# Performance work log

Measured on AMD Instinct MI355X. Metric: run time of the kernel, lower is better.

Reference implementation:

```python
import jax, jax.numpy as jnp
import numpy as np

B, T, D, H = 2, 2048, 2048, 16
HD = D // H  # head_dim = 128


def setup_inputs() -> dict:
    key = jax.random.key(0)
    ks = jax.random.split(key, 7)
    s = 1.0 / np.sqrt(D)
    return {
        "x": jax.random.normal(ks[0], (B, T, D), jnp.float32),
        "Wq": jax.random.normal(ks[1], (D, D), jnp.float32) * s,
        "Wk": jax.random.normal(ks[2], (D, D), jnp.float32) * s,
        "Wv": jax.random.normal(ks[3], (D, D), jnp.float32) * s,
        "Wo": jax.random.normal(ks[4], (D, D), jnp.float32) * s,
        "rope_cos": jax.random.uniform(ks[5], (T, HD), jnp.float32, -1.0, 1.0),
        "rope_sin": jax.random.uniform(ks[6], (T, HD), jnp.float32, -1.0, 1.0),
    }


def _rope(x, cos, sin):
    # x: [B,H,T,HD]; cos/sin: [T,HD] broadcast over batch/heads
    half = x.shape[-1] // 2
    lhs, rhs = x[..., :half], x[..., half:]
    rotated = jnp.concatenate((-rhs, lhs), axis=-1)
    return cos[None, None] * x + rotated * sin[None, None]


def reference(x, Wq, Wk, Wv, Wo, rope_cos, rope_sin):
    Bc, Tc, Dc = x.shape
    # torch nn.Linear: y = x @ W.T
    q = (x @ Wq.T).reshape(Bc, Tc, H, HD).transpose(0, 2, 1, 3)
    k = (x @ Wk.T).reshape(Bc, Tc, H, HD).transpose(0, 2, 1, 3)
    v = (x @ Wv.T).reshape(Bc, Tc, H, HD).transpose(0, 2, 1, 3)
    q = _rope(q, rope_cos[:Tc], rope_sin[:Tc])
    k = _rope(k, rope_cos[:Tc], rope_sin[:Tc])
    scores = jnp.einsum('bhqd,bhkd->bhqk', q, k) / jnp.sqrt(jnp.float32(HD))
    causal = jnp.triu(jnp.ones((Tc, Tc), bool), k=1)
    scores = jnp.where(causal[None, None], -jnp.inf, scores)
    attn = jax.nn.softmax(scores, axis=-1)
    ctx = jnp.einsum('bhqk,bhkd->bhqd', attn, v)
    ctx = ctx.transpose(0, 2, 1, 3).reshape(Bc, Tc, Dc)
    return ctx @ Wo.T
```

## Files before the change

kernel.cpp:

```cpp
#include <hip/hip_runtime.h>

typedef __attribute__((ext_vector_type(4))) float   f32x4;
typedef __attribute__((ext_vector_type(8))) __bf16  bf16x8;
typedef __attribute__((ext_vector_type(4))) __bf16  bf16x4;
typedef __attribute__((ext_vector_type(8))) unsigned short u16x8;

#define NH   16
#define HD   128
#define TSEQ 2048
#define DM   2048
#define MT   4096

__device__ __forceinline__ f32x4 mfma_bf16(bf16x8 a, bf16x8 b, f32x4 c) {
  return __builtin_amdgcn_mfma_f32_16x16x32_bf16(a, b, c, 0, 0, 0);
}

__device__ __forceinline__ void gl_lds16(const __bf16* g, __bf16* l) {
  __builtin_amdgcn_global_load_lds(
      (const __attribute__((address_space(1))) void*)g,
      (__attribute__((address_space(3))) void*)l, 16, 0, 0);
}

__global__ __launch_bounds__(256) void k_cvt(const float* __restrict__ s,
                                             __bf16* __restrict__ d, int n4) {
  int i = blockIdx.x * 256 + threadIdx.x;
  int stride = gridDim.x * 256;
  for (; i < n4; i += stride) {
    f32x4 v = ((const f32x4*)s)[i];
    bf16x4 o;
    o[0] = (__bf16)v[0]; o[1] = (__bf16)v[1];
    o[2] = (__bf16)v[2]; o[3] = (__bf16)v[3];
    ((bf16x4*)d)[i] = o;
  }
}

__global__ __launch_bounds__(256) void k_cvtw(
    const float* __restrict__ W0, const float* __restrict__ W1,
    const float* __restrict__ W2, const float* __restrict__ W3,
    __bf16* __restrict__ D0, __bf16* __restrict__ D1,
    __bf16* __restrict__ D2, __bf16* __restrict__ D3, int n4) {
  int z = blockIdx.z;
  const float* s = (z == 0) ? W0 : (z == 1) ? W1 : (z == 2) ? W2 : W3;
  __bf16*      d = (z == 0) ? D0 : (z == 1) ? D1 : (z == 2) ? D2 : D3;
  int i = blockIdx.x * 256 + threadIdx.x;
  int stride = gridDim.x * 256;
  for (; i < n4; i += stride) {
    f32x4 v = ((const f32x4*)s)[i];
    bf16x4 o;
    o[0] = (__bf16)v[0]; o[1] = (__bf16)v[1];
    o[2] = (__bf16)v[2]; o[3] = (__bf16)v[3];
    ((bf16x4*)d)[i] = o;
  }
}

template <int MODE>
__global__ __launch_bounds__(256) void k_gemm(
    const __bf16* __restrict__ A,
    const __bf16* __restrict__ B0, const __bf16* __restrict__ B1,
    const __bf16* __restrict__ B2,
    __bf16* __restrict__ D0, __bf16* __restrict__ D1, __bf16* __restrict__ D2,
    float* __restrict__ F) {
  __shared__ __bf16 As[128 * 32];
  __shared__ __bf16 Bs[128 * 32];

  const __bf16* __restrict__ Bm;
  __bf16* Dst = nullptr;
  if (MODE == 1) {
    int z = blockIdx.z;
    Bm  = (z == 0) ? B0 : (z == 1 ? B1 : B2);
    Dst = (z == 0) ? D0 : (z == 1 ? D1 : D2);
  } else {
    Bm = B0;
  }

  const int bid = blockIdx.x;
  const int wg  = (bid & 7) * 64 + (bid >> 3);
  const int n0  = (wg & 15) * 128;
  const int m0  = (wg >> 4) * 128;

  const int tid  = threadIdx.x;
  const int lane = tid & 63, w = tid >> 6;
  const int g    = lane >> 4, li = lane & 15;
  const int wr   = w >> 1, wc = w & 1;
  const int srow = lane >> 2;
  const int sseg = lane & 3;

  const f32x4 zero = {0.f, 0.f, 0.f, 0.f};
  f32x4 acc[4][4];
#pragma unroll
  for (int i = 0; i < 4; i++)
#pragma unroll
    for (int j = 0; j < 4; j++) acc[i][j] = zero;

  for (int k0 = 0; k0 < DM; k0 += 32) {
#pragma unroll
    for (int c = 0; c < 2; c++) {
      const int ch = w * 2 + c;
      gl_lds16(&A[(size_t)(m0 + ch * 16 + srow) * DM + k0 + sseg * 8],
               &As[ch * 512]);
      gl_lds16(&Bm[(size_t)(n0 + ch * 16 + srow) * DM + k0 + sseg * 8],
               &Bs[ch * 512]);
    }
    __syncthreads();
    bf16x8 af[4], bfr[4];
#pragma unroll
    for (int i = 0; i < 4; i++)
      af[i] = *(const bf16x8*)&As[(wr * 64 + i * 16 + li) * 32 + g * 8];
#pragma unroll
    for (int i = 0; i < 4; i++)
      bfr[i] = *(const bf16x8*)&Bs[(wc * 64 + i * 16 + li) * 32 + g * 8];
#pragma unroll
    for (int mi = 0; mi < 4; mi++)
#pragma unroll
      for (int ni = 0; ni < 4; ni++)
        acc[mi][ni] = mfma_bf16(af[mi], bfr[ni], acc[mi][ni]);
    __syncthreads();
  }

#pragma unroll
  for (int mi = 0; mi < 4; mi++)
#pragma unroll
    for (int ni = 0; ni < 4; ni++) {
      int colb = n0 + wc * 64 + ni * 16 + li;
#pragma unroll
      for (int r = 0; r < 4; r++) {
        int rowb = m0 + wr * 64 + mi * 16 + g * 4 + r;
        float vv = acc[mi][ni][r];
        if (MODE == 0) {
          F[(size_t)rowb * DM + colb] = vv;
        } else {
          int h = colb >> 7, d = colb & 127;
          int b = rowb >> 11, t = rowb & 2047;
          Dst[(((size_t)(b * NH + h)) * TSEQ + t) * HD + d] = (__bf16)vv;
        }
      }
    }
}

__global__ __launch_bounds__(256) void k_rope(__bf16* __restrict__ q,
                                              __bf16* __restrict__ kk,
                                              const float* __restrict__ rc,
                                              const float* __restrict__ rs) {
  int gid    = blockIdx.x * 256 + threadIdx.x;
  int tensor = gid >> 20;
  int rem    = gid & ((1 << 20) - 1);
  int bh     = rem >> 15;
  int r2     = rem & 32767;
  int t      = r2 >> 4;
  int j      = r2 & 15;
  int d0     = j * 4;
  __bf16* base = (tensor ? kk : q) + ((size_t)bh * TSEQ + t) * HD;
  f32x4 ca = *(const f32x4*)&rc[t * HD + d0];
  f32x4 cb = *(const f32x4*)&rc[t * HD + d0 + 64];
  f32x4 sa = *(const f32x4*)&rs[t * HD + d0];
  f32x4 sb = *(const f32x4*)&rs[t * HD + d0 + 64];
  bf16x4 xa = *(bf16x4*)&base[d0];
  bf16x4 xb = *(bf16x4*)&base[d0 + 64];
  bf16x4 oa, ob;
#pragma unroll
  for (int u = 0; u < 4; u++) {
    float fa = (float)xa[u], fb = (float)xb[u];
    oa[u] = (__bf16)(ca[u] * fa - fb * sa[u]);
    ob[u] = (__bf16)(cb[u] * fb + fa * sb[u]);
  }
  *(bf16x4*)&base[d0]      = oa;
  *(bf16x4*)&base[d0 + 64] = ob;
}

__global__ __launch_bounds__(256) void k_trans(const __bf16* __restrict__ v,
                                               __bf16* __restrict__ vt) {
  __shared__ unsigned short tile[64][73];
  int bh = blockIdx.z;
  int t0 = blockIdx.x * 64, d0 = blockIdx.y * 64;
  int tid = threadIdx.x;
  int r = tid >> 2, s4 = tid & 3;
  const unsigned short* src =
      (const unsigned short*)v + ((size_t)bh * TSEQ + t0) * HD + d0;
  u16x8 a = *(const u16x8*)&src[(size_t)r * HD + s4 * 16];
  u16x8 b = *(const u16x8*)&src[(size_t)r * HD + s4 * 16 + 8];
#pragma unroll
  for (int u = 0; u < 8; u++) {
    tile[r][s4 * 16 + u]     = a[u];
    tile[r][s4 * 16 + 8 + u] = b[u];
  }
  __syncthreads();
  unsigned short* dst =
      (unsigned short*)vt + ((size_t)bh * HD + d0) * TSEQ + t0;
  u16x8 o1, o2;
#pragma unroll
  for (int u = 0; u < 8; u++) {
    o1[u] = tile[s4 * 16 + u][r];
    o2[u] = tile[s4 * 16 + 8 + u][r];
  }
  *(u16x8*)&dst[(size_t)r * TSEQ + s4 * 16]     = o1;
  *(u16x8*)&dst[(size_t)r * TSEQ + s4 * 16 + 8] = o2;
}

__global__ __launch_bounds__(256, 2) void k_attn(const __bf16* __restrict__ q,
                                                 const __bf16* __restrict__ k,
                                                 const __bf16* __restrict__ vt,
                                                 __bf16* __restrict__ ctx) {
  __shared__ __bf16 Ks[64 * 136];
  __shared__ __bf16 Vs[128 * 72];
  __shared__ __bf16 Ps[4][32 * 72];

  const int bid = blockIdx.x;
  const int wg  = (bid & 7) * 64 + (bid >> 3);
  const int bh  = wg >> 4;
  const int qt  = 15 - (wg & 15);
  const int q0  = qt * 128;

  const int tid  = threadIdx.x;
  const int lane = tid & 63, w = tid >> 6;
  const int g    = lane >> 4, li = lane & 15;
  const int qw   = q0 + w * 32;

  const __bf16* qb = q  + (size_t)bh * TSEQ * HD;
  const __bf16* kb = k  + (size_t)bh * TSEQ * HD;
  const __bf16* vb = vt + (size_t)bh * HD * TSEQ;

  const float CST = 0.08838834764831845f * 1.4426950408889634f;
  bf16x8 qf[2][4];
#pragma unroll
  for (int s = 0; s < 2; s++)
#pragma unroll
    for (int kc = 0; kc < 4; kc++) {
      bf16x8 t =
          *(const bf16x8*)&qb[(size_t)(qw + s * 16 + li) * HD + kc * 32 + g * 8];
      bf16x8 o;
#pragma unroll
      for (int e = 0; e < 8; e++) o[e] = (__bf16)((float)t[e] * CST);
      qf[s][kc] = o;
    }

  const f32x4 zero = {0.f, 0.f, 0.f, 0.f};
  f32x4 o[2][8];
#pragma unroll
  for (int s = 0; s < 2; s++)
#pragma unroll
    for (int dt = 0; dt < 8; dt++) o[s][dt] = zero;
  float mrow[2][4], lrow[2][4];
#pragma unroll
  for (int s = 0; s < 2; s++)
#pragma unroll
    for (int r = 0; r < 4; r++) { mrow[s][r] = -1e30f; lrow[s][r] = 0.f; }

  const int nkt = 2 * qt + 2;

  const int kR = tid >> 4, kS = tid & 15;
  const int vR = tid >> 3, vS = tid & 7;

  bf16x8 pk[4], pv[4];
#pragma unroll
  for (int i = 0; i < 4; i++) {
    pk[i] = *(const bf16x8*)&kb[(size_t)(kR + 16 * i) * HD + kS * 8];
    pv[i] = *(const bf16x8*)&vb[(size_t)(vR + 32 * i) * TSEQ + vS * 8];
  }

  for (int kt = 0; kt < nkt; kt++) {
    const int kv0 = kt * 64;
    __syncthreads();
#pragma unroll
    for (int i = 0; i < 4; i++)
      *(bf16x8*)&Ks[(kR + 16 * i) * 136 + kS * 8] = pk[i];
#pragma unroll
    for (int i = 0; i < 4; i++)
      *(bf16x8*)&Vs[(vR + 32 * i) * 72 + vS * 8] = pv[i];
    if (kt + 1 < nkt) {
      const int nv0 = kv0 + 64;
#pragma unroll
      for (int i = 0; i < 4; i++) {
        pk[i] = *(const bf16x8*)&kb[(size_t)(nv0 + kR + 16 * i) * HD + kS * 8];
        pv[i] = *(const bf16x8*)&vb[(size_t)(vR + 32 * i) * TSEQ + nv0 + vS * 8];
      }
    }
    __syncthreads();

    if (kv0 <= qw + 31) {
      f32x4 sc[2][4];
#pragma unroll
      for (int s = 0; s < 2; s++)
#pragma unroll
        for (int kvf = 0; kvf < 4; kvf++) sc[s][kvf] = zero;
#pragma unroll
      for (int kvf = 0; kvf < 4; kvf++)
#pragma unroll
        for (int kc = 0; kc < 4; kc++) {
          bf16x8 kf =
              *(const bf16x8*)&Ks[(kvf * 16 + li) * 136 + kc * 32 + g * 8];
          sc[0][kvf] = mfma_bf16(qf[0][kc], kf, sc[0][kvf]);
          sc[1][kvf] = mfma_bf16(qf[1][kc], kf, sc[1][kvf]);
        }
      if (kv0 + 63 > qw) {
#pragma unroll
        for (int s = 0; s < 2; s++)
#pragma unroll
          for (int kvf = 0; kvf < 4; kvf++) {
            int kg = kv0 + kvf * 16 + li;
#pragma unroll
            for (int r = 0; r < 4; r++) {
              int qg = qw + s * 16 + g * 4 + r;
              if (kg > qg) sc[s][kvf][r] = -1e30f;
            }
          }
      }
      float mnew[2][4];
      bool upd = false;
#pragma unroll
      for (int s = 0; s < 2; s++)
#pragma unroll
        for (int r = 0; r < 4; r++) {
          float a = fmaxf(fmaxf(sc[s][0][r], sc[s][1][r]),
                          fmaxf(sc[s][2][r], sc[s][3][r]));
          a = fmaxf(a, __shfl_xor(a, 1));
          a = fmaxf(a, __shfl_xor(a, 2));
          a = fmaxf(a, __shfl_xor(a, 4));
          a = fmaxf(a, __shfl_xor(a, 8));
          mnew[s][r] = fmaxf(mrow[s][r], a);
          upd = upd || (a > mrow[s][r]);
        }
      if (__any(upd)) {
#pragma unroll
        for (int s = 0; s < 2; s++)
#pragma unroll
          for (int r = 0; r < 4; r++) {
            float fac = __builtin_amdgcn_exp2f(mrow[s][r] - mnew[s][r]);
            mrow[s][r] = mnew[s][r];
            lrow[s][r] *= fac;
#pragma unroll
            for (int dt = 0; dt < 8; dt++) o[s][dt][r] *= fac;
          }
      }
#pragma unroll
      for (int s = 0; s < 2; s++)
#pragma unroll
        for (int kvf = 0; kvf < 4; kvf++) {
#pragma unroll
          for (int r = 0; r < 4; r++) {
            float p = __builtin_amdgcn_exp2f(sc[s][kvf][r] - mrow[s][r]);
            lrow[s][r] += p;
            Ps[w][(s * 16 + g * 4 + r) * 72 + kvf * 16 + li] = (__bf16)p;
          }
        }
      bf16x8 pa[2][2];
#pragma unroll
      for (int s = 0; s < 2; s++)
#pragma unroll
        for (int kvs = 0; kvs < 2; kvs++)
          pa[s][kvs] =
              *(const bf16x8*)&Ps[w][(s * 16 + li) * 72 + kvs * 32 + g * 8];
#pragma unroll
      for (int dt = 0; dt < 8; dt++) {
        bf16x8 v0 = *(const bf16x8*)&Vs[(dt * 16 + li) * 72 + g * 8];
        bf16x8 v1 = *(const bf16x8*)&Vs[(dt * 16 + li) * 72 + 32 + g * 8];
        o[0][dt] = mfma_bf16(pa[0][0], v0, o[0][dt]);
        o[0][dt] = mfma_bf16(pa[0][1], v1, o[0][dt]);
        o[1][dt] = mfma_bf16(pa[1][0], v0, o[1][dt]);
        o[1][dt] = mfma_bf16(pa[1][1], v1, o[1][dt]);
      }
    }
  }

  const int b = bh >> 4, h = bh & 15;
#pragma unroll
  for (int s = 0; s < 2; s++)
#pragma unroll
    for (int r = 0; r < 4; r++) {
      float l = lrow[s][r];
      l += __shfl_xor(l, 1);
      l += __shfl_xor(l, 2);
      l += __shfl_xor(l, 4);
      l += __shfl_xor(l, 8);
      float inv = 1.0f / l;
      size_t rowoff =
          ((size_t)(b * TSEQ + qw + s * 16 + g * 4 + r)) * DM + h * HD;
#pragma unroll
      for (int dt = 0; dt < 8; dt++)
        ctx[rowoff + dt * 16 + li] = (__bf16)(o[s][dt][r] * inv);
    }
}

extern "C" void kernel_launch(void* const* d_in, const int* in_sizes, int n_in,
                              void* d_out, int out_size, void* d_ws,
                              size_t ws_size, hipStream_t stream) {
  const float* x  = (const float*)d_in[0];
  const float* Wq = (const float*)d_in[1];
  const float* Wk = (const float*)d_in[2];
  const float* Wv = (const float*)d_in[3];
  const float* Wo = (const float*)d_in[4];
  const float* rc = (const float*)d_in[5];
  const float* rs = (const float*)d_in[6];
  float* out = (float*)d_out;

  __bf16* xb   = (__bf16*)d_ws;
  __bf16* wqb  = xb  + (size_t)MT * DM;
  __bf16* wkb  = wqb + (size_t)DM * DM;
  __bf16* wvb  = wkb + (size_t)DM * DM;
  __bf16* wob  = wvb + (size_t)DM * DM;
  __bf16* qbuf = wob + (size_t)DM * DM;
  __bf16* kbuf = qbuf + (size_t)MT * DM;
  __bf16* vbuf = kbuf + (size_t)MT * DM;
  __bf16* vtb  = vbuf + (size_t)MT * DM;
  __bf16* ctxb = vbuf;

  k_cvt<<<2048, 256, 0, stream>>>(x, xb, (MT * DM) / 4);
  dim3 gw(1024, 1, 4);
  k_cvtw<<<gw, 256, 0, stream>>>(Wq, Wk, Wv, Wo, wqb, wkb, wvb, wob,
                                 (DM * DM) / 4);

  dim3 gqkv(512, 1, 3);
  k_gemm<1><<<gqkv, 256, 0, stream>>>(xb, wqb, wkb, wvb, qbuf, kbuf, vbuf,
                                      nullptr);
  k_rope<<<8192, 256, 0, stream>>>(qbuf, kbuf, rc, rs);

  dim3 gt(TSEQ / 64, HD / 64, 32);
  k_trans<<<gt, 256, 0, stream>>>(vbuf, vtb);

  k_attn<<<512, 256, 0, stream>>>(qbuf, kbuf, vtb, ctxb);

  dim3 go(512, 1, 1);
  k_gemm<0><<<go, 256, 0, stream>>>(ctxb, wob, nullptr, nullptr, nullptr,
                                    nullptr, nullptr, out);
}
```

Before: 440.8 us.

## Use 256x256 double-buffered swizzled GEMM for QKV projection and merge conversions

Replaces the 128x128 single-buffered QKV projection GEMM with a 512-thread 256x256-tile kernel. It uses BK=64, double-buffered LDS loaded via global_load_lds, an XOR swizzle against bank conflicts, and s_setprio around the MFMA phases. The x conversion is folded into the weight conversion launch as a fifth z-slice, saving one launch. The output projection keeps the old kernel, now specialised. The larger tile gives more reuse per byte loaded and overlaps loads with compute, but gives only 384 blocks and 128KB of LDS per block, which limits occupancy.

```diff
diff --git a/kernel.cpp b/kernel.cpp
--- a/kernel.cpp
+++ b/kernel.cpp
@@ -10,6 +10,7 @@
 #define TSEQ 2048
 #define DM   2048
 #define MT   4096
+#define NT   (DM / 64)
 
 __device__ __forceinline__ f32x4 mfma_bf16(bf16x8 a, bf16x8 b, f32x4 c) {
   return __builtin_amdgcn_mfma_f32_16x16x32_bf16(a, b, c, 0, 0, 0);
@@ -21,8 +22,19 @@
       (__attribute__((address_space(3))) void*)l, 16, 0, 0);
 }
 
-__global__ __launch_bounds__(256) void k_cvt(const float* __restrict__ s,
-                                             __bf16* __restrict__ d, int n4) {
+__global__ __launch_bounds__(256) void k_cvtw(
+    const float* __restrict__ X,
+    const float* __restrict__ W0, const float* __restrict__ W1,
+    const float* __restrict__ W2, const float* __restrict__ W3,
+    __bf16* __restrict__ DX,
+    __bf16* __restrict__ D0, __bf16* __restrict__ D1,
+    __bf16* __restrict__ D2, __bf16* __restrict__ D3) {
+  int z = blockIdx.z;
+  const float* s = (z == 0) ? W0 : (z == 1) ? W1 : (z == 2) ? W2
+                   : (z == 3) ? W3 : X;
+  __bf16*      d = (z == 0) ? D0 : (z == 1) ? D1 : (z == 2) ? D2
+                   : (z == 3) ? D3 : DX;
+  int n4 = (z == 4) ? (MT * DM / 4) : (DM * DM / 4);
   int i = blockIdx.x * 256 + threadIdx.x;
   int stride = gridDim.x * 256;
   for (; i < n4; i += stride) {
@@ -34,44 +46,122 @@
   }
 }
 
-__global__ __launch_bounds__(256) void k_cvtw(
-    const float* __restrict__ W0, const float* __restrict__ W1,
-    const float* __restrict__ W2, const float* __restrict__ W3,
-    __bf16* __restrict__ D0, __bf16* __restrict__ D1,
-    __bf16* __restrict__ D2, __bf16* __restrict__ D3, int n4) {
-  int z = blockIdx.z;
-  const float* s = (z == 0) ? W0 : (z == 1) ? W1 : (z == 2) ? W2 : W3;
-  __bf16*      d = (z == 0) ? D0 : (z == 1) ? D1 : (z == 2) ? D2 : D3;
-  int i = blockIdx.x * 256 + threadIdx.x;
-  int stride = gridDim.x * 256;
-  for (; i < n4; i += stride) {
-    f32x4 v = ((const f32x4*)s)[i];
-    bf16x4 o;
-    o[0] = (__bf16)v[0]; o[1] = (__bf16)v[1];
-    o[2] = (__bf16)v[2]; o[3] = (__bf16)v[3];
-    ((bf16x4*)d)[i] = o;
-  }
-}
-
-template <int MODE>
-__global__ __launch_bounds__(256) void k_gemm(
+__global__ __launch_bounds__(512, 2) void k_gemm256(
     const __bf16* __restrict__ A,
     const __bf16* __restrict__ B0, const __bf16* __restrict__ B1,
     const __bf16* __restrict__ B2,
-    __bf16* __restrict__ D0, __bf16* __restrict__ D1, __bf16* __restrict__ D2,
-    float* __restrict__ F) {
+    __bf16* __restrict__ D0, __bf16* __restrict__ D1,
+    __bf16* __restrict__ D2) {
+  __shared__ __bf16 lds[2][2][16384];
+
+  const int z = blockIdx.z;
+  const __bf16* __restrict__ Bm = (z == 0) ? B0 : (z == 1 ? B1 : B2);
+  __bf16* Dst = (z == 0) ? D0 : (z == 1 ? D1 : D2);
+
+  const int bid = blockIdx.x;
+  const int wg  = (bid & 7) * 16 + (bid >> 3);
+  const int m0  = (wg >> 3) * 256;
+  const int n0  = (wg & 7) * 256;
+
+  const int tid  = threadIdx.x;
+  const int lane = tid & 63, w = tid >> 6;
+  const int wr   = w >> 2, wc = w & 3;
+  const int g    = lane >> 4, li = lane & 15;
+
+  const __bf16* __restrict__ Ap = A + (size_t)m0 * DM;
+  const __bf16* __restrict__ Bp = Bm + (size_t)n0 * DM;
+
+  const int srow = w * 8 + (lane >> 3);
+  const int scol = ((lane & 7) * 8) ^ (((lane >> 3) & 3) << 4);
+
+#define STAGE256(WB, KT)                                                     \
+  {                                                                          \
+    const int k1_ = (KT) * 64;                                               \
+    _Pragma("unroll") for (int ht = 0; ht < 4; ht++) {                       \
+      const __bf16* sp_ = (ht < 2) ? Ap : Bp;                                \
+      const int hf_ = ht & 1;                                                \
+      _Pragma("unroll") for (int qq = 0; qq < 2; qq++) {                     \
+        gl_lds16(&sp_[(size_t)(hf_ * 128 + qq * 64 + srow) * DM + k1_ + scol],\
+                 &lds[WB][ht >> 1][hf_ * 8192 + qq * 4096 + w * 512]);       \
+      }                                                                      \
+    }                                                                        \
+  }
+
+  const f32x4 zero = {0.f, 0.f, 0.f, 0.f};
+  f32x4 acc[8][4];
+#pragma unroll
+  for (int i = 0; i < 8; i++)
+#pragma unroll
+    for (int j = 0; j < 4; j++) acc[i][j] = zero;
+
+#define QPHASE(RD, MQ, NQ)                                                   \
+  {                                                                          \
+    bf16x8 af_[4][2], bf_[2][2];                                             \
+    _Pragma("unroll") for (int i = 0; i < 4; i++)                            \
+      _Pragma("unroll") for (int kk = 0; kk < 2; kk++) {                     \
+        const int rl_ = MQ * 64 + i * 16 + li;                               \
+        af_[i][kk] = *(const bf16x8*)&lds[RD][0][                            \
+            wr * 8192 + rl_ * 64 + ((kk * 32 + g * 8) ^ ((li & 3) << 4))];   \
+      }                                                                      \
+    _Pragma("unroll") for (int j = 0; j < 2; j++)                            \
+      _Pragma("unroll") for (int kk = 0; kk < 2; kk++) {                     \
+        const int rb_ = wc * 64 + NQ * 32 + j * 16 + li;                     \
+        bf_[j][kk] = *(const bf16x8*)&lds[RD][1][                            \
+            (rb_ >> 7) * 8192 + (rb_ & 127) * 64 +                           \
+            ((kk * 32 + g * 8) ^ ((li & 3) << 4))];                          \
+      }                                                                      \
+    __builtin_amdgcn_s_setprio(1);                                           \
+    _Pragma("unroll") for (int i = 0; i < 4; i++)                            \
+      _Pragma("unroll") for (int j = 0; j < 2; j++)                          \
+        _Pragma("unroll") for (int kk = 0; kk < 2; kk++)                     \
+          acc[MQ * 4 + i][NQ * 2 + j] =                                      \
+              mfma_bf16(af_[i][kk], bf_[j][kk], acc[MQ * 4 + i][NQ * 2 + j]);\
+    __builtin_amdgcn_s_setprio(0);                                           \
+    __builtin_amdgcn_s_barrier();                                            \
+  }
+
+  STAGE256(0, 0);
+  asm volatile("s_waitcnt vmcnt(0)" ::: "memory");
+  __builtin_amdgcn_s_barrier();
+
+  for (int t = 0; t < NT; ++t) {
+    const int rd = t & 1;
+    if (t + 1 < NT) {
+      if (rd == 0) STAGE256(1, t + 1) else STAGE256(0, t + 1);
+    }
+    if (rd == 0) {
+      QPHASE(0, 0, 0); QPHASE(0, 0, 1); QPHASE(0, 1, 0); QPHASE(0, 1, 1);
+    } else {
+      QPHASE(1, 0, 0); QPHASE(1, 0, 1); QPHASE(1, 1, 0); QPHASE(1, 1, 1);
+    }
+    asm volatile("s_waitcnt vmcnt(0)" ::: "memory");
+    __builtin_amdgcn_s_barrier();
+  }
+
+#pragma unroll
+  for (int i = 0; i < 8; i++) {
+#pragma unroll
+    for (int j = 0; j < 4; j++) {
+      const int col = n0 + wc * 64 + j * 16 + li;
+      const int h = col >> 7, d = col & 127;
+#pragma unroll
+      for (int r = 0; r < 4; r++) {
+        const int row = m0 + wr * 128 + i * 16 + g * 4 + r;
+        const int b = row >> 11, t = row & 2047;
+        Dst[(((size_t)(b * NH + h)) * TSEQ + t) * HD + d] =
+            (__bf16)acc[i][j][r];
+      }
+    }
+  }
+#undef STAGE256
+#undef QPHASE
+}
+
+__global__ __launch_bounds__(256) void k_gemm_o(const __bf16* __restrict__ A,
+                                                const __bf16* __restrict__ Bm,
+                                                float* __restrict__ F) {
   __shared__ __bf16 As[128 * 32];
   __shared__ __bf16 Bs[128 * 32];
-
-  const __bf16* __restrict__ Bm;
-  __bf16* Dst = nullptr;
-  if (MODE == 1) {
-    int z = blockIdx.z;
-    Bm  = (z == 0) ? B0 : (z == 1 ? B1 : B2);
-    Dst = (z == 0) ? D0 : (z == 1 ? D1 : D2);
-  } else {
-    Bm = B0;
-  }
 
   const int bid = blockIdx.x;
   const int wg  = (bid & 7) * 64 + (bid >> 3);
@@ -125,14 +215,7 @@
 #pragma unroll
       for (int r = 0; r < 4; r++) {
         int rowb = m0 + wr * 64 + mi * 16 + g * 4 + r;
-        float vv = acc[mi][ni][r];
-        if (MODE == 0) {
-          F[(size_t)rowb * DM + colb] = vv;
-        } else {
-          int h = colb >> 7, d = colb & 127;
-          int b = rowb >> 11, t = rowb & 2047;
-          Dst[(((size_t)(b * NH + h)) * TSEQ + t) * HD + d] = (__bf16)vv;
-        }
+        F[(size_t)rowb * DM + colb] = acc[mi][ni][r];
       }
     }
 }
@@ -403,14 +486,12 @@
   __bf16* vtb  = vbuf + (size_t)MT * DM;
   __bf16* ctxb = vbuf;
 
-  k_cvt<<<2048, 256, 0, stream>>>(x, xb, (MT * DM) / 4);
-  dim3 gw(1024, 1, 4);
-  k_cvtw<<<gw, 256, 0, stream>>>(Wq, Wk, Wv, Wo, wqb, wkb, wvb, wob,
-                                 (DM * DM) / 4);
-
-  dim3 gqkv(512, 1, 3);
-  k_gemm<1><<<gqkv, 256, 0, stream>>>(xb, wqb, wkb, wvb, qbuf, kbuf, vbuf,
-                                      nullptr);
+  dim3 gw(1024, 1, 5);
+  k_cvtw<<<gw, 256, 0, stream>>>(x, Wq, Wk, Wv, Wo, xb, wqb, wkb, wvb, wob);
+
+  dim3 gqkv(128, 1, 3);
+  k_gemm256<<<gqkv, 512, 0, stream>>>(xb, wqb, wkb, wvb, qbuf, kbuf, vbuf);
+
   k_rope<<<8192, 256, 0, stream>>>(qbuf, kbuf, rc, rs);
 
   dim3 gt(TSEQ / 64, HD / 64, 32);
@@ -418,7 +499,5 @@
 
   k_attn<<<512, 256, 0, stream>>>(qbuf, kbuf, vtb, ctxb);
 
-  dim3 go(512, 1, 1);
-  k_gemm<0><<<go, 256, 0, stream>>>(ctxb, wob, nullptr, nullptr, nullptr,
-                                    nullptr, nullptr, out);
-}
+  k_gemm_o<<<512, 256, 0, stream>>>(ctxb, wob, out);
+}
```

New measurement: 906.7 us. 2.06x slower.
